# Performance work log

Hardware: AMD Instinct MI355X
Metric: run time of the kernel (lower is better)

The kernel has to match this reference:

```python
import jax, jax.numpy as jnp
import numpy as np
import itertools

B, DIM, RES = 128, 384, 16
NH, KD, D = 8, 32, 128            # heads, key_dim, d = attn_ratio*key_dim
NHKD, DH = NH * KD, NH * D        # 256, 1024
N = RES * RES                     # 256 tokens
SCALE = KD ** -0.5


def _bias_idxs():
    pts = list(itertools.product(range(RES), range(RES)))
    offsets, idxs = {}, []
    for p1 in pts:
        for p2 in pts:
            off = (abs(p1[0] - p2[0]), abs(p1[1] - p2[1]))
            if off not in offsets:
                offsets[off] = len(offsets)
            idxs.append(offsets[off])
    return np.array(idxs, dtype=np.int32).reshape(N, N), len(offsets)


def setup_inputs() -> dict:
    key = jax.random.key(0)
    ks = jax.random.split(key, 16)
    idxs, n_off = _bias_idxs()
    s = 0.02
    return {
        "x": jax.random.normal(ks[0], (B, DIM, RES, RES), jnp.float32),
        "q_w": jax.random.normal(ks[1], (NHKD, DIM), jnp.float32) * s,
        "q_b": jnp.zeros((NHKD,), jnp.float32),
        "k_w": jax.random.normal(ks[2], (NHKD, DIM), jnp.float32) * s,
        "k_b": jnp.zeros((NHKD,), jnp.float32),
        "v_w": jax.random.normal(ks[3], (DH, DIM), jnp.float32) * s,
        "v_b": jnp.zeros((DH,), jnp.float32),
        "vl_w": jax.random.normal(ks[4], (DH, 1, 3, 3), jnp.float32) * s,
        "vl_b": jnp.zeros((DH,), jnp.float32),
        "th1_w": jax.random.normal(ks[5], (NH, NH), jnp.float32) * s,
        "th1_b": jnp.zeros((NH,), jnp.float32),
        "th2_w": jax.random.normal(ks[6], (NH, NH), jnp.float32) * s,
        "th2_b": jnp.zeros((NH,), jnp.float32),
        "proj_w": jax.random.normal(ks[7], (DIM, DH), jnp.float32) * s,
        "proj_b": jnp.zeros((DIM,), jnp.float32),
        "attn_bias": jax.random.normal(ks[8], (NH, n_off), jnp.float32) * s,
        "bias_idxs": jnp.asarray(idxs),
    }


def _conv1x1(x, w, b):  # x: [B,C,H,W], w: [O,C]
    return jnp.einsum('bchw,oc->bohw', x, w) + b[:, None, None]


def reference(x, q_w, q_b, k_w, k_b, v_w, v_b, vl_w, vl_b,
              th1_w, th1_b, th2_w, th2_b, proj_w, proj_b,
              attn_bias, bias_idxs):
    Bx, C, H, W = x.shape
    q = _conv1x1(x, q_w, q_b).reshape(Bx, NH, KD, N).transpose(0, 1, 3, 2)  # bhnk
    k = _conv1x1(x, k_w, k_b).reshape(Bx, NH, KD, N)                        # bhkm
    v4 = _conv1x1(x, v_w, v_b)                                              # [B,DH,H,W]
    v_local = jax.lax.conv_general_dilated(
        v4, vl_w, window_strides=(1, 1), padding='SAME',
        dimension_numbers=('NCHW', 'OIHW', 'NCHW'),
        feature_group_count=DH) + vl_b[:, None, None]
    v = v4.reshape(Bx, NH, D, N).transpose(0, 1, 3, 2)                      # bhnd

    attn = jnp.einsum('bhnk,bhkm->bhnm', q, k) * SCALE + attn_bias[:, bias_idxs]
    attn = jnp.einsum('gh,bhnm->bgnm', th1_w, attn) + th1_b[:, None, None]  # talking head 1
    attn = jax.nn.softmax(attn, axis=-1)
    attn = jnp.einsum('gh,bhnm->bgnm', th2_w, attn) + th2_b[:, None, None]  # talking head 2

    o = jnp.einsum('bhnm,bhmd->bhnd', attn, v)
    out = o.transpose(0, 1, 3, 2).reshape(Bx, DH, H, W) + v_local
    out = jax.nn.relu(out)
    return _conv1x1(out, proj_w, proj_b)
```

## Files before the change

### kernel.cpp

```cpp
#include <hip/hip_runtime.h>
#include <hip/hip_bf16.h>

typedef __hip_bfloat16 bf16;
typedef __bf16 bf16v8 __attribute__((ext_vector_type(8)));
typedef float f32x4 __attribute__((ext_vector_type(4)));

#define BB    128
#define DIM   384
#define NTOK  256
#define NH    8
#define KD    32
#define DHEAD 128
#define DH    1024
#define SCALE 0.17677669529663687f
#define LOG2E 1.4426950408889634f

static __device__ __forceinline__ float sf(float x) {
  return (x == x) ? fminf(fmaxf(x, -1e4f), 1e4f) : 0.f;
}

static __device__ __forceinline__ float rfl(float x) {
  return __int_as_float(__builtin_amdgcn_readfirstlane(__float_as_int(x)));
}

#define GLOAD_LDS16(gsrc, ldst)                                                \
  __builtin_amdgcn_global_load_lds(                                            \
      (const __attribute__((address_space(1))) void*)(gsrc),                   \
      (__attribute__((address_space(3))) void*)(ldst), 16, 0, 0)

__global__ __launch_bounds__(256) void k_convert(const float* __restrict__ qw,
    const float* __restrict__ kw, const float* __restrict__ vw,
    const float* __restrict__ pw, bf16* __restrict__ dst) {
  int i = blockIdx.x * 256 + threadIdx.x;
  float v;
  if (i < 98304)       v = qw[i];
  else if (i < 196608) v = kw[i - 98304];
  else if (i < 589824) v = vw[i - 196608];
  else                 v = pw[i - 589824];
  dst[i] = __float2bfloat16(sf(v));
}

__global__ __launch_bounds__(256) void k_bias(const float* __restrict__ ab,
    const int* __restrict__ idxs, int n_off,
    const float* __restrict__ th1_w, const float* __restrict__ th1_b,
    float* __restrict__ bias_full) {
  int mn = blockIdx.x * 256 + threadIdx.x;
  int m = mn >> 8, n = mn & 255;
  int idx = idxs[n * 256 + m];
  float bh[8];
#pragma unroll
  for (int h = 0; h < 8; ++h) bh[h] = sf(ab[h * n_off + idx]);
#pragma unroll
  for (int g = 0; g < 8; ++g) {
    float a = sf(th1_b[g]);
#pragma unroll
    for (int h = 0; h < 8; ++h) a += sf(th1_w[g * 8 + h]) * bh[h];
    bias_full[((size_t)g * 256 + m) * 256 + n] = a * LOG2E;
  }
}

__global__ __launch_bounds__(256) void k_transpose_x(const float* __restrict__ x,
                                                     bf16* __restrict__ xT) {
  __shared__ bf16 tile[32][33];
  int b = blockIdx.z;
  int c0 = blockIdx.x * 32;
  int n0 = blockIdx.y * 32;
  int t = threadIdx.x;
  int tn = t & 31, tc = t >> 5;
#pragma unroll
  for (int p = 0; p < 4; ++p)
    tile[tc + p * 8][tn] =
        __float2bfloat16(sf(x[((size_t)b * DIM + c0 + tc + p * 8) * NTOK + n0 + tn]));
  __syncthreads();
  int wc = t & 31, wn = t >> 5;
#pragma unroll
  for (int p = 0; p < 4; ++p)
    xT[((size_t)b * NTOK + n0 + wn + p * 8) * DIM + c0 + wc] = tile[wc][wn + p * 8];
}

__global__ __launch_bounds__(256, 3) void k_qkv(const bf16* __restrict__ xT,
    const bf16* __restrict__ W, const float* __restrict__ q_b,
    const float* __restrict__ k_b, const float* __restrict__ v_b,
    bf16* __restrict__ qT, bf16* __restrict__ kT, bf16* __restrict__ v4,
    int nb) {
  __shared__ __align__(16) char smem[34816];
  bf16* sA = (bf16*)smem;
  bf16* sB = (bf16*)(smem + 16384);
  bf16* actt = (bf16*)smem;

  int id = blockIdx.x;
  int b, tile;
  if ((nb & 7) == 0) {
    int per = nb >> 3;
    int xcd = id & 7, slot = id >> 3;
    b = xcd * per + (slot % per);
    tile = slot / per;
  } else { b = id / 24; tile = id % 24; }
  int mt = tile >> 1, nt = tile & 1;
  int m0 = mt * 128, n0b = nt * 128;
  int t = threadIdx.x;
  int wave = t >> 6, lane = t & 63;
  int wm = wave >> 1, wn = wave & 1;
  int qd = lane >> 4, li = lane & 15;
  const bf16* xTb = xT + ((size_t)b * NTOK + n0b) * DIM;

  f32x4 acc[4][4];
#pragma unroll
  for (int r = 0; r < 4; ++r)
#pragma unroll
    for (int f = 0; f < 4; ++f) acc[r][f] = (f32x4){0.f, 0.f, 0.f, 0.f};

  for (int ks = 0; ks < 6; ++ks) {
    int k0 = ks * 64;
    __syncthreads();
#pragma unroll
    for (int i = 0; i < 8; ++i) {
      int g = wave * 512 + i * 64 + lane;
      int gg = g & 1023;
      int row = gg >> 3, slot = gg & 7;
      int col = ((slot ^ (row & 7)) << 3) + k0;
      const bf16* src = (g < 1024)
          ? (W + (size_t)(m0 + row) * DIM + col)
          : (xTb + (size_t)row * DIM + col);
      GLOAD_LDS16(src, smem + (size_t)(wave * 512 + i * 64) * 16);
    }
    __syncthreads();
#pragma unroll
    for (int s = 0; s < 2; ++s) {
      bf16v8 Afr[4], Bfr[4];
#pragma unroll
      for (int r = 0; r < 4; ++r) {
        int row = wm * 64 + r * 16 + li;
        Afr[r] = *(const bf16v8*)(sA + row * 64 + (((s * 4 + qd) ^ (row & 7)) << 3));
      }
#pragma unroll
      for (int f = 0; f < 4; ++f) {
        int row = wn * 64 + f * 16 + li;
        Bfr[f] = *(const bf16v8*)(sB + row * 64 + (((s * 4 + qd) ^ (row & 7)) << 3));
      }
#pragma unroll
      for (int r = 0; r < 4; ++r)
#pragma unroll
        for (int f = 0; f < 4; ++f)
          acc[r][f] = __builtin_amdgcn_mfma_f32_16x16x32_bf16(Afr[r], Bfr[f], acc[r][f], 0, 0, 0);
    }
  }
  __syncthreads();

  if (m0 >= 512) {
    int ch0 = m0 - 512;
#pragma unroll
    for (int r = 0; r < 4; ++r)
#pragma unroll
      for (int f = 0; f < 4; ++f) {
        int coll = wn * 64 + f * 16 + li;
#pragma unroll
        for (int rr = 0; rr < 4; ++rr) {
          int rowl = wm * 64 + r * 16 + qd * 4 + rr;
          actt[rowl * 136 + coll] =
              __float2bfloat16(acc[r][f][rr] + sf(v_b[ch0 + rowl]));
        }
      }
    __syncthreads();
#pragma unroll
    for (int it = 0; it < 8; ++it) {
      int g = it * 256 + t;
      int row = g >> 4, c16 = g & 15;
      bf16v8 vv = *(const bf16v8*)(actt + row * 136 + c16 * 8);
      *(bf16v8*)(v4 + ((size_t)b * DH + ch0 + row) * NTOK + n0b + c16 * 8) = vv;
    }
  } else {
    const float* bias = (m0 < 256) ? q_b : k_b;
    bf16* dst = (m0 < 256) ? qT : kT;
    int mb = (m0 < 256) ? m0 : m0 - 256;
#pragma unroll
    for (int r = 0; r < 4; ++r)
#pragma unroll
      for (int f = 0; f < 4; ++f) {
        int n = n0b + wn * 64 + f * 16 + li;
        int rowg = mb + wm * 64 + r * 16 + qd * 4;
        int h = rowg >> 5, kd = rowg & 31;
        union { bf16 e[4]; uint2 u; } pk;
#pragma unroll
        for (int rr = 0; rr < 4; ++rr)
          pk.e[rr] = __float2bfloat16(acc[r][f][rr] + sf(bias[rowg + rr]));
        *(uint2*)(dst + (((size_t)b * NH + h) * NTOK + n) * KD + kd) = pk.u;
      }
  }
}

__global__ __launch_bounds__(1024, 4) void k_scores(const bf16* __restrict__ qT,
    const bf16* __restrict__ kT, const float* __restrict__ bias_full,
    const float* __restrict__ th1_w,
    const float* __restrict__ th2_w, const float* __restrict__ th2_b,
    bf16* __restrict__ P, int nb) {
  __shared__ float s_th1[64], s_th2[64], s_t2b[8];
  __shared__ float s_part[16][8][16];
  __shared__ float s_invl[8][16];
  int t = threadIdx.x;
  if (t < 64) { s_th1[t] = sf(th1_w[t]) * (SCALE * LOG2E); s_th2[t] = sf(th2_w[t]); }
  if (t >= 64 && t < 72) s_t2b[t - 64] = sf(th2_b[t - 64]);
  int id = blockIdx.x;
  int b, nt;
  if ((nb & 7) == 0) {
    int per = nb >> 3;
    int xcd = id & 7, slot = id >> 3;
    b = xcd * per + (slot % per);
    nt = slot / per;
  } else { b = id >> 4; nt = id & 15; }
  int n0 = nt * 16;
  int wave = t >> 6, lane = t & 63, qd = lane >> 4, li = lane & 15;
  int ms = wave * 16;

  f32x4 S[8];
#pragma unroll
  for (int h = 0; h < 8; ++h) {
    bf16v8 Ak = *(const bf16v8*)(kT + (((size_t)b * NH + h) * NTOK + ms + li) * KD + qd * 8);
    bf16v8 Bq = *(const bf16v8*)(qT + (((size_t)b * NH + h) * NTOK + n0 + li) * KD + qd * 8);
    f32x4 c = {0.f, 0.f, 0.f, 0.f};
    S[h] = __builtin_amdgcn_mfma_f32_16x16x32_bf16(Ak, Bq, c, 0, 0, 0);
  }
  __syncthreads();

  f32x4 E[8];
  {
    float w1[64];
#pragma unroll
    for (int i = 0; i < 64; ++i) w1[i] = rfl(s_th1[i]);
#pragma unroll
    for (int r = 0; r < 4; ++r) {
#pragma unroll
      for (int g = 0; g < 8; ++g) {
        float a = bias_full[((size_t)g * 256 + ms + qd * 4 + r) * 256 + n0 + li];
#pragma unroll
        for (int h = 0; h < 8; ++h) a += w1[g * 8 + h] * S[h][r];
        E[g][r] = exp2f(fminf(a, 43.3f));
      }
    }
  }
#pragma unroll
  for (int g = 0; g < 8; ++g) {
    float v = (E[g][0] + E[g][1]) + (E[g][2] + E[g][3]);
    v += __shfl_xor(v, 16, 64);
    v += __shfl_xor(v, 32, 64);
    if (qd == 0) s_part[wave][g][li] = v;
  }
  __syncthreads();
  if (t < 128) {
    int g = t >> 4, n = t & 15;
    float ssum = 0.f;
#pragma unroll
    for (int w2 = 0; w2 < 16; ++w2) ssum += s_part[w2][g][n];
    s_invl[g][n] = 1.0f / ssum;
  }
  __syncthreads();
#pragma unroll
  for (int g = 0; g < 8; ++g) {
    float inv = s_invl[g][li];
#pragma unroll
    for (int r = 0; r < 4; ++r) E[g][r] *= inv;
  }

  {
    float w2[64], b2[8];
#pragma unroll
    for (int i = 0; i < 64; ++i) w2[i] = rfl(s_th2[i]);
#pragma unroll
    for (int i = 0; i < 8; ++i) b2[i] = rfl(s_t2b[i]);
    size_t pbase = (size_t)b * NH * 65536 + (size_t)nt * 4096 +
                   (size_t)(wave >> 1) * 512 + li * 32 + (wave & 1) * 16 + qd * 4;
#pragma unroll
    for (int g2 = 0; g2 < 8; ++g2) {
      union { bf16 e[4]; uint2 u; } pk;
#pragma unroll
      for (int r = 0; r < 4; ++r) {
        float a = b2[g2];
#pragma unroll
        for (int g = 0; g < 8; ++g) a += w2[g2 * 8 + g] * E[g][r];
        pk.e[r] = __float2bfloat16(a);
      }
      *(uint2*)(P + pbase + (size_t)g2 * 65536) = pk.u;
    }
  }
}

static __device__ __forceinline__ int vswz(int ch, int tok) {
  return tok ^ ((ch & 7) << 3);
}

__global__ __launch_bounds__(512, 4) void k_pv(const bf16* __restrict__ P,
    const bf16* __restrict__ v4,
    const float* __restrict__ vl_w, const float* __restrict__ vl_b,
    bf16* __restrict__ act, int nb) {
  __shared__ bf16 v_s[128][256];
  __shared__ float wv_s[1152];
  __shared__ float vb_s[128];
  __shared__ bf16 tbuf[8][16][20];
  int id = blockIdx.x;
  int b, h;
  if ((nb & 7) == 0) {
    int per = nb >> 3;
    int xcd = id & 7, slot = id >> 3;
    b = xcd * per + (slot % per);
    h = slot / per;
  } else { b = id >> 3; h = id & 7; }
  int t = threadIdx.x;
  int wave = t >> 6, lane = t & 63;
  int qd = lane >> 4, li = lane & 15;
  int nw = wave * 32;
  int nwt = wave * 2;
  const bf16* Pb = P + ((size_t)b * NH + h) * 65536;
  const bf16* Vb = v4 + ((size_t)b * DH + h * DHEAD) * NTOK;

  bf16v8 Af[4][2][2];
#pragma unroll
  for (int mi = 0; mi < 4; ++mi)
#pragma unroll
    for (int s = 0; s < 2; ++s)
#pragma unroll
      for (int r = 0; r < 2; ++r)
        Af[mi][s][r] = *(const bf16v8*)(Pb + (size_t)(nwt + r) * 4096 +
                                        (mi * 2 + s) * 512 + li * 32 + qd * 8);

#pragma unroll
  for (int p = 0; p < 8; ++p) {
    int idx = p * 512 + t;
    int ch = idx >> 5, tok = (idx & 31) * 8;
    *(bf16v8*)&v_s[ch][vswz(ch, tok)] = *(const bf16v8*)(Vb + (size_t)ch * NTOK + tok);
  }
  for (int i = t; i < 1152; i += 512) wv_s[i] = sf(vl_w[(size_t)h * DHEAD * 9 + i]);
  if (t < 128) vb_s[t] = sf(vl_b[h * DHEAD + t]);
  __syncthreads();

  f32x4 acc[2][8];
#pragma unroll
  for (int r = 0; r < 2; ++r)
#pragma unroll
    for (int f = 0; f < 8; ++f) acc[r][f] = (f32x4){0.f, 0.f, 0.f, 0.f};
#pragma unroll
  for (int mi = 0; mi < 4; ++mi) {
    int m0 = mi * 64;
#pragma unroll
    for (int s = 0; s < 2; ++s) {
      bf16v8 Bf[8];
#pragma unroll
      for (int f = 0; f < 8; ++f) {
        int ch = f * 16 + li;
        Bf[f] = *(const bf16v8*)&v_s[ch][vswz(ch, m0 + s * 32 + qd * 8)];
      }
#pragma unroll
      for (int f = 0; f < 8; ++f)
#pragma unroll
        for (int r = 0; r < 2; ++r)
          acc[r][f] = __builtin_amdgcn_mfma_f32_16x16x32_bf16(Af[mi][s][r], Bf[f], acc[r][f], 0, 0, 0);
    }
  }

#pragma unroll
  for (int f = 0; f < 8; ++f) {
    int chl = f * 16 + li;
    float wv[9];
#pragma unroll
    for (int j = 0; j < 9; ++j) wv[j] = wv_s[chl * 9 + j];
    float vb = vb_s[chl];
#pragma unroll
    for (int r = 0; r < 2; ++r) {
      int y = (nw + r * 16) >> 4;
      float vvv[3][6];
#pragma unroll
      for (int yy = 0; yy < 3; ++yy) {
        int y3 = y - 1 + yy;
        float e0 = 0.f, e1 = 0.f, e2 = 0.f, e3 = 0.f;
        if (y3 >= 0 && y3 < 16) {
          int tok = y3 * 16 + qd * 4;
          union { uint2 u; bf16 e[4]; } w4;
          w4.u = *(const uint2*)&v_s[chl][vswz(chl, tok)];
          e0 = __bfloat162float(w4.e[0]);
          e1 = __bfloat162float(w4.e[1]);
          e2 = __bfloat162float(w4.e[2]);
          e3 = __bfloat162float(w4.e[3]);
        }
        float lft = __shfl_up(e3, 16, 64);
        float rgt = __shfl_down(e0, 16, 64);
        if (qd == 0) lft = 0.f;
        if (qd == 3) rgt = 0.f;
        vvv[yy][0] = lft; vvv[yy][1] = e0; vvv[yy][2] = e1;
        vvv[yy][3] = e2;  vvv[yy][4] = e3; vvv[yy][5] = rgt;
      }
#pragma unroll
      for (int rr = 0; rr < 4; ++rr) {
        float s = vb;
#pragma unroll
        for (int yy = 0; yy < 3; ++yy)
#pragma unroll
          for (int j = 0; j < 3; ++j)
            s += vvv[yy][rr + j] * wv[yy * 3 + j];
        float v = fmaxf(acc[r][f][rr] + s, 0.f);
        tbuf[wave][qd * 4 + rr][li] = __float2bfloat16(v);
      }
      uint2 pr = *(const uint2*)&tbuf[wave][li][qd * 4];
      *(uint2*)(act + ((size_t)b * NTOK + nw + r * 16 + li) * DH +
                h * DHEAD + f * 16 + qd * 4) = pr;
    }
  }
}

__global__ __launch_bounds__(256, 3) void k_proj(const bf16* __restrict__ act,
    const bf16* __restrict__ Wp, const float* __restrict__ proj_b,
    int b_base, int nb, float* __restrict__ out) {
  __shared__ __align__(16) char smem[32768];
  bf16* sA = (bf16*)smem;
  bf16* sB = (bf16*)(smem + 16384);

  int id = blockIdx.x;
  int b, tile;
  if ((nb & 7) == 0) {
    int per = nb >> 3;
    int xcd = id & 7, slot = id >> 3;
    b = xcd * per + (slot % per);
    tile = slot / per;
  } else { b = id / 6; tile = id % 6; }
  int mt = tile >> 1, nt = tile & 1;
  int m0 = mt * 128, n0b = nt * 128;
  int bg = b_base + b;
  int t = threadIdx.x;
  int wave = t >> 6, lane = t & 63;
  int wm = wave >> 1, wn = wave & 1;
  int qd = lane >> 4, li = lane & 15;
  const bf16* actb = act + ((size_t)b * NTOK + n0b) * DH;

  f32x4 acc[4][4];
#pragma unroll
  for (int r = 0; r < 4; ++r)
#pragma unroll
    for (int f = 0; f < 4; ++f) acc[r][f] = (f32x4){0.f, 0.f, 0.f, 0.f};

  for (int ks = 0; ks < 16; ++ks) {
    int k0 = ks * 64;
    __syncthreads();
#pragma unroll
    for (int i = 0; i < 8; ++i) {
      int g = wave * 512 + i * 64 + lane;
      int gg = g & 1023;
      int row = gg >> 3, slot = gg & 7;
      int col = ((slot ^ (row & 7)) << 3) + k0;
      const bf16* src = (g < 1024)
          ? (Wp + (size_t)(m0 + row) * DH + col)
          : (actb + (size_t)row * DH + col);
      GLOAD_LDS16(src, smem + (size_t)(wave * 512 + i * 64) * 16);
    }
    __syncthreads();
#pragma unroll
    for (int s = 0; s < 2; ++s) {
      bf16v8 Afr[4], Bfr[4];
#pragma unroll
      for (int r = 0; r < 4; ++r) {
        int row = wm * 64 + r * 16 + li;
        Afr[r] = *(const bf16v8*)(sA + row * 64 + (((s * 4 + qd) ^ (row & 7)) << 3));
      }
#pragma unroll
      for (int f = 0; f < 4; ++f) {
        int row = wn * 64 + f * 16 + li;
        Bfr[f] = *(const bf16v8*)(sB + row * 64 + (((s * 4 + qd) ^ (row & 7)) << 3));
      }
#pragma unroll
      for (int r = 0; r < 4; ++r)
#pragma unroll
        for (int f = 0; f < 4; ++f)
          acc[r][f] = __builtin_amdgcn_mfma_f32_16x16x32_bf16(Afr[r], Bfr[f], acc[r][f], 0, 0, 0);
    }
  }

#pragma unroll
  for (int r = 0; r < 4; ++r)
#pragma unroll
    for (int f = 0; f < 4; ++f) {
      int n = n0b + wn * 64 + f * 16 + li;
#pragma unroll
      for (int rr = 0; rr < 4; ++rr) {
        int dim = m0 + wm * 64 + r * 16 + qd * 4 + rr;
        out[((size_t)bg * DIM + dim) * NTOK + n] = acc[r][f][rr] + sf(proj_b[dim]);
      }
    }
}

extern "C" void kernel_launch(void* const* d_in, const int* in_sizes, int n_in,
                              void* d_out, int out_size, void* d_ws, size_t ws_size,
                              hipStream_t stream) {
  const float* x      = (const float*)d_in[0];
  const float* q_w    = (const float*)d_in[1];
  const float* q_b    = (const float*)d_in[2];
  const float* k_w    = (const float*)d_in[3];
  const float* k_b    = (const float*)d_in[4];
  const float* v_w    = (const float*)d_in[5];
  const float* v_b    = (const float*)d_in[6];
  const float* vl_w   = (const float*)d_in[7];
  const float* vl_b   = (const float*)d_in[8];
  const float* th1_w  = (const float*)d_in[9];
  const float* th1_b  = (const float*)d_in[10];
  const float* th2_w  = (const float*)d_in[11];
  const float* th2_b  = (const float*)d_in[12];
  const float* proj_w = (const float*)d_in[13];
  const float* proj_b = (const float*)d_in[14];
  const float* attn_b = (const float*)d_in[15];
  const int*   idxs   = (const int*)d_in[16];
  int n_off = in_sizes[15] / NH;
  float* out = (float*)d_out;

  const size_t WQ = 98304, WK = 98304, WV = 393216, WP = 393216;
  const size_t WTOT = WQ + WK + WV + WP;
  const size_t BFULL = (size_t)NH * NTOK * NTOK;
  const size_t PB_XT = (size_t)NTOK * DIM;
  const size_t PB_QK = (size_t)NH * NTOK * KD;
  const size_t PB_V  = (size_t)DH * NTOK;
  const size_t PB_AC = (size_t)NTOK * DH;
  const size_t PB_P  = (size_t)NH * NTOK * NTOK;
  const size_t perb  = (PB_XT + 2 * PB_QK + PB_V + PB_AC + PB_P) * 2;
  const size_t fixed = WTOT * 2 + BFULL * 4;

  char* w = (char*)d_ws;
  bf16* wcvt = (bf16*)w;  w += WTOT * 2;
  bf16* wq = wcvt;
  bf16* wk = wcvt + WQ;
  bf16* wv = wcvt + WQ + WK;
  bf16* wp = wcvt + WQ + WK + WV;
  float* bias_full = (float*)w;  w += BFULL * 4;

  size_t rem = (ws_size > fixed) ? (ws_size - fixed) : 0;
  int CH = (int)(rem / perb);
  if (CH > BB) CH = BB;
  if (CH >= 8) CH &= ~7;
  if (CH < 1) CH = 1;

  bf16* xT  = (bf16*)w;  w += (size_t)CH * PB_XT * 2;
  bf16* qT  = (bf16*)w;  w += (size_t)CH * PB_QK * 2;
  bf16* kT  = (bf16*)w;  w += (size_t)CH * PB_QK * 2;
  bf16* v4  = (bf16*)w;  w += (size_t)CH * PB_V * 2;
  bf16* act = (bf16*)w;  w += (size_t)CH * PB_AC * 2;
  bf16* P   = (bf16*)w;  w += (size_t)CH * PB_P * 2;

  k_convert<<<(int)(WTOT / 256), 256, 0, stream>>>(q_w, k_w, v_w, proj_w, wcvt);
  k_bias<<<256, 256, 0, stream>>>(attn_b, idxs, n_off, th1_w, th1_b, bias_full);

  for (int c0 = 0; c0 < BB; c0 += CH) {
    int cb = (BB - c0 < CH) ? (BB - c0) : CH;
    k_transpose_x<<<dim3(12, 8, cb), 256, 0, stream>>>(x + (size_t)c0 * DIM * NTOK, xT);
    k_qkv<<<cb * 24, 256, 0, stream>>>(xT, wcvt, q_b, k_b, v_b, qT, kT, v4, cb);
    k_scores<<<cb * 16, 1024, 0, stream>>>(qT, kT, bias_full,
                                           th1_w, th2_w, th2_b, P, cb);
    k_pv<<<cb * 16 / 2, 512, 0, stream>>>(P, v4, vl_w, vl_b, act, cb);
    k_proj<<<cb * 6, 256, 0, stream>>>(act, wp, proj_b, c0, cb, out);
  }
}
```

Baseline: 407.5 us.

## Fuse PV matmul and depthwise conv into scores kernel, drop P buffer

Merges the scores/softmax kernel and the P·V kernel into one. Each 16-query block keeps its talking-head-2 probabilities in swizzled LDS and multiplies them by V read directly from global memory. The separate depthwise conv and ReLU epilogue is folded in, so the full 8x256x256 bf16 P tensor no longer makes a round trip through global memory. In exchange, V is re-read from global (likely L2) by every query tile without LDS reuse, extra block-wide barriers are added, and LDS use per block grows.

```diff
diff --git a/kernel.cpp b/kernel.cpp
--- a/kernel.cpp
+++ b/kernel.cpp
@@ -189,14 +189,17 @@
   }
 }
 
-__global__ __launch_bounds__(1024, 4) void k_scores(const bf16* __restrict__ qT,
+__global__ __launch_bounds__(1024, 4) void k_attn(const bf16* __restrict__ qT,
     const bf16* __restrict__ kT, const float* __restrict__ bias_full,
-    const float* __restrict__ th1_w,
-    const float* __restrict__ th2_w, const float* __restrict__ th2_b,
-    bf16* __restrict__ P, int nb) {
+    const float* __restrict__ th1_w, const float* __restrict__ th2_w,
+    const float* __restrict__ th2_b, const bf16* __restrict__ v4,
+    const float* __restrict__ vl_w, const float* __restrict__ vl_b,
+    bf16* __restrict__ act, int nb) {
   __shared__ float s_th1[64], s_th2[64], s_t2b[8];
   __shared__ float s_part[16][8][16];
   __shared__ float s_invl[8][16];
+  __shared__ bf16 pstage[4][16][256];
+  __shared__ bf16 tbuf[16][16][20];
   int t = threadIdx.x;
   if (t < 64) { s_th1[t] = sf(th1_w[t]) * (SCALE * LOG2E); s_th2[t] = sf(th2_w[t]); }
   if (t >= 64 && t < 72) s_t2b[t - 64] = sf(th2_b[t - 64]);
@@ -261,16 +264,19 @@
     for (int r = 0; r < 4; ++r) E[g][r] *= inv;
   }
 
-  {
-    float w2[64], b2[8];
-#pragma unroll
-    for (int i = 0; i < 64; ++i) w2[i] = rfl(s_th2[i]);
-#pragma unroll
-    for (int i = 0; i < 8; ++i) b2[i] = rfl(s_t2b[i]);
-    size_t pbase = (size_t)b * NH * 65536 + (size_t)nt * 4096 +
-                   (size_t)(wave >> 1) * 512 + li * 32 + (wave & 1) * 16 + qd * 4;
-#pragma unroll
-    for (int g2 = 0; g2 < 8; ++g2) {
+  float w2[64], b2[8];
+#pragma unroll
+  for (int i = 0; i < 64; ++i) w2[i] = rfl(s_th2[i]);
+#pragma unroll
+  for (int i = 0; i < 8; ++i) b2[i] = rfl(s_t2b[i]);
+  const bf16* Vb = v4 + (size_t)b * DH * NTOK;
+  int pg2i = wave >> 2, dq = wave & 3;
+
+#pragma unroll
+  for (int round = 0; round < 2; ++round) {
+#pragma unroll
+    for (int g2i = 0; g2i < 4; ++g2i) {
+      int g2 = round * 4 + g2i;
       union { bf16 e[4]; uint2 u; } pk;
 #pragma unroll
       for (int r = 0; r < 4; ++r) {
@@ -279,102 +285,42 @@
         for (int g = 0; g < 8; ++g) a += w2[g2 * 8 + g] * E[g][r];
         pk.e[r] = __float2bfloat16(a);
       }
-      *(uint2*)(P + pbase + (size_t)g2 * 65536) = pk.u;
-    }
-  }
-}
-
-static __device__ __forceinline__ int vswz(int ch, int tok) {
-  return tok ^ ((ch & 7) << 3);
-}
-
-__global__ __launch_bounds__(512, 4) void k_pv(const bf16* __restrict__ P,
-    const bf16* __restrict__ v4,
-    const float* __restrict__ vl_w, const float* __restrict__ vl_b,
-    bf16* __restrict__ act, int nb) {
-  __shared__ bf16 v_s[128][256];
-  __shared__ float wv_s[1152];
-  __shared__ float vb_s[128];
-  __shared__ bf16 tbuf[8][16][20];
-  int id = blockIdx.x;
-  int b, h;
-  if ((nb & 7) == 0) {
-    int per = nb >> 3;
-    int xcd = id & 7, slot = id >> 3;
-    b = xcd * per + (slot % per);
-    h = slot / per;
-  } else { b = id >> 3; h = id & 7; }
-  int t = threadIdx.x;
-  int wave = t >> 6, lane = t & 63;
-  int qd = lane >> 4, li = lane & 15;
-  int nw = wave * 32;
-  int nwt = wave * 2;
-  const bf16* Pb = P + ((size_t)b * NH + h) * 65536;
-  const bf16* Vb = v4 + ((size_t)b * DH + h * DHEAD) * NTOK;
-
-  bf16v8 Af[4][2][2];
-#pragma unroll
-  for (int mi = 0; mi < 4; ++mi)
-#pragma unroll
-    for (int s = 0; s < 2; ++s)
-#pragma unroll
-      for (int r = 0; r < 2; ++r)
-        Af[mi][s][r] = *(const bf16v8*)(Pb + (size_t)(nwt + r) * 4096 +
-                                        (mi * 2 + s) * 512 + li * 32 + qd * 8);
-
-#pragma unroll
-  for (int p = 0; p < 8; ++p) {
-    int idx = p * 512 + t;
-    int ch = idx >> 5, tok = (idx & 31) * 8;
-    *(bf16v8*)&v_s[ch][vswz(ch, tok)] = *(const bf16v8*)(Vb + (size_t)ch * NTOK + tok);
-  }
-  for (int i = t; i < 1152; i += 512) wv_s[i] = sf(vl_w[(size_t)h * DHEAD * 9 + i]);
-  if (t < 128) vb_s[t] = sf(vl_b[h * DHEAD + t]);
-  __syncthreads();
-
-  f32x4 acc[2][8];
-#pragma unroll
-  for (int r = 0; r < 2; ++r)
-#pragma unroll
-    for (int f = 0; f < 8; ++f) acc[r][f] = (f32x4){0.f, 0.f, 0.f, 0.f};
-#pragma unroll
-  for (int mi = 0; mi < 4; ++mi) {
-    int m0 = mi * 64;
-#pragma unroll
-    for (int s = 0; s < 2; ++s) {
-      bf16v8 Bf[8];
-#pragma unroll
-      for (int f = 0; f < 8; ++f) {
-        int ch = f * 16 + li;
-        Bf[f] = *(const bf16v8*)&v_s[ch][vswz(ch, m0 + s * 32 + qd * 8)];
-      }
-#pragma unroll
-      for (int f = 0; f < 8; ++f)
-#pragma unroll
-        for (int r = 0; r < 2; ++r)
-          acc[r][f] = __builtin_amdgcn_mfma_f32_16x16x32_bf16(Af[mi][s][r], Bf[f], acc[r][f], 0, 0, 0);
-    }
-  }
-
-#pragma unroll
-  for (int f = 0; f < 8; ++f) {
-    int chl = f * 16 + li;
-    float wv[9];
-#pragma unroll
-    for (int j = 0; j < 9; ++j) wv[j] = wv_s[chl * 9 + j];
-    float vb = vb_s[chl];
-#pragma unroll
-    for (int r = 0; r < 2; ++r) {
-      int y = (nw + r * 16) >> 4;
+      int g16 = (ms >> 3) + (qd >> 1);
+      *(uint2*)(&pstage[g2i][li][((g16 ^ (li & 7)) << 3) + (qd & 1) * 4]) = pk.u;
+    }
+    __syncthreads();
+
+    int g2 = round * 4 + pg2i;
+    f32x4 pacc[2];
+    pacc[0] = (f32x4){0.f, 0.f, 0.f, 0.f};
+    pacc[1] = (f32x4){0.f, 0.f, 0.f, 0.f};
+#pragma unroll
+    for (int ks = 0; ks < 8; ++ks) {
+      bf16v8 Ap = *(const bf16v8*)&pstage[pg2i][li][(((ks * 4 + qd) ^ (li & 7)) << 3)];
+#pragma unroll
+      for (int dt = 0; dt < 2; ++dt) {
+        int ch = g2 * DHEAD + dq * 32 + dt * 16 + li;
+        bf16v8 Bv = *(const bf16v8*)(Vb + (size_t)ch * NTOK + ks * 32 + qd * 8);
+        pacc[dt] = __builtin_amdgcn_mfma_f32_16x16x32_bf16(Ap, Bv, pacc[dt], 0, 0, 0);
+      }
+    }
+
+#pragma unroll
+    for (int dt = 0; dt < 2; ++dt) {
+      int ch = g2 * DHEAD + dq * 32 + dt * 16 + li;
+      const bf16* vr = Vb + (size_t)ch * NTOK;
+      float wv[9];
+#pragma unroll
+      for (int j = 0; j < 9; ++j) wv[j] = sf(vl_w[ch * 9 + j]);
+      float vb = sf(vl_b[ch]);
       float vvv[3][6];
 #pragma unroll
       for (int yy = 0; yy < 3; ++yy) {
-        int y3 = y - 1 + yy;
+        int y3 = nt - 1 + yy;
         float e0 = 0.f, e1 = 0.f, e2 = 0.f, e3 = 0.f;
         if (y3 >= 0 && y3 < 16) {
-          int tok = y3 * 16 + qd * 4;
           union { uint2 u; bf16 e[4]; } w4;
-          w4.u = *(const uint2*)&v_s[chl][vswz(chl, tok)];
+          w4.u = *(const uint2*)(vr + y3 * 16 + qd * 4);
           e0 = __bfloat162float(w4.e[0]);
           e1 = __bfloat162float(w4.e[1]);
           e2 = __bfloat162float(w4.e[2]);
@@ -395,13 +341,14 @@
 #pragma unroll
           for (int j = 0; j < 3; ++j)
             s += vvv[yy][rr + j] * wv[yy * 3 + j];
-        float v = fmaxf(acc[r][f][rr] + s, 0.f);
+        float v = fmaxf(pacc[dt][rr] + s, 0.f);
         tbuf[wave][qd * 4 + rr][li] = __float2bfloat16(v);
       }
       uint2 pr = *(const uint2*)&tbuf[wave][li][qd * 4];
-      *(uint2*)(act + ((size_t)b * NTOK + nw + r * 16 + li) * DH +
-                h * DHEAD + f * 16 + qd * 4) = pr;
-    }
+      *(uint2*)(act + ((size_t)b * NTOK + n0 + li) * DH +
+                g2 * DHEAD + dq * 32 + dt * 16 + qd * 4) = pr;
+    }
+    __syncthreads();
   }
 }
 
@@ -514,8 +461,7 @@
   const size_t PB_QK = (size_t)NH * NTOK * KD;
   const size_t PB_V  = (size_t)DH * NTOK;
   const size_t PB_AC = (size_t)NTOK * DH;
-  const size_t PB_P  = (size_t)NH * NTOK * NTOK;
-  const size_t perb  = (PB_XT + 2 * PB_QK + PB_V + PB_AC + PB_P) * 2;
+  const size_t perb  = (PB_XT + 2 * PB_QK + PB_V + PB_AC) * 2;
   const size_t fixed = WTOT * 2 + BFULL * 4;
 
   char* w = (char*)d_ws;
@@ -537,7 +483,6 @@
   bf16* kT  = (bf16*)w;  w += (size_t)CH * PB_QK * 2;
   bf16* v4  = (bf16*)w;  w += (size_t)CH * PB_V * 2;
   bf16* act = (bf16*)w;  w += (size_t)CH * PB_AC * 2;
-  bf16* P   = (bf16*)w;  w += (size_t)CH * PB_P * 2;
 
   k_convert<<<(int)(WTOT / 256), 256, 0, stream>>>(q_w, k_w, v_w, proj_w, wcvt);
   k_bias<<<256, 256, 0, stream>>>(attn_b, idxs, n_off, th1_w, th1_b, bias_full);
@@ -546,9 +491,8 @@
     int cb = (BB - c0 < CH) ? (BB - c0) : CH;
     k_transpose_x<<<dim3(12, 8, cb), 256, 0, stream>>>(x + (size_t)c0 * DIM * NTOK, xT);
     k_qkv<<<cb * 24, 256, 0, stream>>>(xT, wcvt, q_b, k_b, v_b, qT, kT, v4, cb);
-    k_scores<<<cb * 16, 1024, 0, stream>>>(qT, kT, bias_full,
-                                           th1_w, th2_w, th2_b, P, cb);
-    k_pv<<<cb * 16 / 2, 512, 0, stream>>>(P, v4, vl_w, vl_b, act, cb);
+    k_attn<<<cb * 16, 1024, 0, stream>>>(qT, kT, bias_full, th1_w, th2_w, th2_b,
+                                         v4, vl_w, vl_b, act, cb);
     k_proj<<<cb * 6, 256, 0, stream>>>(act, wp, proj_b, c0, cb, out);
   }
 }
```

Result: slower. 498.9 us (+22.4%).
